# Performance work log

Measured on AMD Instinct MI355X. Metric: run time of the kernel, lower is better.

The kernel has to match this reference:

```python
import jax, jax.numpy as jnp
import numpy as np

B, T, H, W, D, NH, DEPTH, NCODES = 2, 16, 16, 16, 512, 8, 6, 1024
HW = H * W; DH = D // NH; KH = KW = 3; SIZE = KH * KW; MLP_DIM = 2 * D
NEG = -1e9


def _ln(x, g, b, eps=1e-5):
    m = jnp.mean(x, -1, keepdims=True)
    v = jnp.mean((x - m) ** 2, -1, keepdims=True)
    return (x - m) * jax.lax.rsqrt(v + eps) * g + b


def _rope(x, pos):
    # x: [N, h, T, dh]; half-split rotary embedding
    half = x.shape[-1] // 2
    freqs = 1.0 / (10000.0 ** (jnp.arange(half, dtype=jnp.float32) / half))
    ang = pos[:, None] * freqs[None]            # [T, half]
    cos = jnp.concatenate([jnp.cos(ang), jnp.cos(ang)], -1)
    sin = jnp.concatenate([jnp.sin(ang), jnp.sin(ang)], -1)
    rot = jnp.concatenate([-x[..., half:], x[..., :half]], -1)
    return x * cos + rot * sin


def setup_inputs() -> dict:
    key = jax.random.key(0)
    keys = iter(jax.random.split(key, 64))
    def p(shape, s=0.02):
        return (s * jax.random.normal(next(keys), shape)).astype(jnp.float32)
    inp = dict(
        codes=jax.random.randint(next(keys), (B, T, HW), 0, NCODES),
        emb_table=p((NCODES, D)),
        cls_token=p((1, 1, 1, D)),
        h_emb=p((1, 1, H, D)),
        w_emb=p((1, 1, W, D)),
        emb_norm_g=jnp.ones(D), emb_norm_b=jnp.zeros(D),
        sn_g=jnp.ones((DEPTH, D)), sn_b=jnp.zeros((DEPTH, D)),
        s_wq=p((DEPTH, D, D)), s_bq=jnp.zeros((DEPTH, D)),
        s_wk=p((DEPTH, D, D)), s_bk=jnp.zeros((DEPTH, D)),
        s_wv=p((DEPTH, D, D)), s_bv=jnp.zeros((DEPTH, D)),
        s_wo=p((DEPTH, D, D)), s_bo=jnp.zeros((DEPTH, D)),
        tn_g=jnp.ones((DEPTH, D)), tn_b=jnp.zeros((DEPTH, D)),
        t_wq=p((DEPTH, D, D)), t_bq=jnp.zeros((DEPTH, D)),
        t_wk=p((DEPTH, D, D)), t_bk=jnp.zeros((DEPTH, D)),
        t_wv=p((DEPTH, D, D)), t_bv=jnp.zeros((DEPTH, D)),
        t_wo=p((DEPTH, D, D)), t_bo=jnp.zeros((DEPTH, D)),
        mn_g=jnp.ones((DEPTH, D)), mn_b=jnp.zeros((DEPTH, D)),
        mlp_w1=p((DEPTH, D, MLP_DIM)), mlp_b1=jnp.zeros((DEPTH, MLP_DIM)),
        mlp_w2=p((DEPTH, MLP_DIM, D)), mlp_b2=jnp.zeros((DEPTH, D)),
        fn_g=jnp.ones(D), fn_b=jnp.zeros(D),
    )
    return inp


def reference(codes, emb_table, cls_token, h_emb, w_emb, emb_norm_g, emb_norm_b,
              sn_g, sn_b, s_wq, s_bq, s_wk, s_bk, s_wv, s_bv, s_wo, s_bo,
              tn_g, tn_b, t_wq, t_bq, t_wk, t_bk, t_wv, t_bv, t_wo, t_bo,
              mn_g, mn_b, mlp_w1, mlp_b1, mlp_w2, mlp_b2, fn_g, fn_b):
    T1 = T + 1
    emb = emb_table[codes]                                   # [B,T,HW,D]
    # positional embeddings exactly as torch repeat / repeat_interleave
    x = emb + jnp.tile(h_emb, (1, 1, W, 1)) + jnp.repeat(w_emb, H, axis=2)
    x = jnp.concatenate([x, jnp.broadcast_to(cls_token, (B, 1, HW, D))], axis=1)
    x = _ln(x, emb_norm_g, emb_norm_b)                       # [B,T1,HW,D]

    # temporal causal mask: True = masked
    tmask = jnp.triu(jnp.ones((T1, T1), dtype=bool), 1).at[-1, -1].set(True)
    # spatial out-of-bounds mask [H,W,SIZE] from unfold of ones with zero pad
    ones_pad = jnp.pad(jnp.ones((H, W), jnp.float32), 1)
    smask = jnp.stack([ones_pad[a:a + H, b:b + W]
                       for a in range(KH) for b in range(KW)], -1) == 0

    scale = 1.0 / jnp.sqrt(jnp.float32(DH))
    pos = jnp.arange(T1, dtype=jnp.float32)
    k_list, v_list = [], []
    attn_logits = None
    for i in range(DEPTH):
        # ---- spatial windowed attention on frames 0..T-1 ----
        xg = x[:, :-1].reshape(B, T, H, W, D)
        xn = _ln(xg, sn_g[i], sn_b[i])
        pad = jnp.pad(xn, ((0, 0), (0, 0), (1, 1), (1, 1), (0, 0)))
        nb = jnp.stack([pad[:, :, a:a + H, b:b + W]
                        for a in range(KH) for b in range(KW)], axis=4)  # [B,T,H,W,SIZE,D]
        q = (xn @ s_wq[i] + s_bq[i]).reshape(B, T, H, W, NH, DH)
        kk = (nb @ s_wk[i] + s_bk[i]).reshape(B, T, H, W, SIZE, NH, DH)
        vv = (nb @ s_wv[i] + s_bv[i]).reshape(B, T, H, W, SIZE, NH, DH)
        lg = jnp.einsum('btxynd,btxysnd->btxyns', q, kk) * scale
        lg = jnp.where(smask[None, None, :, :, None, :], NEG, lg)
        a_sp = jax.nn.softmax(lg, -1)
        o = jnp.einsum('btxyns,btxysnd->btxynd', a_sp, vv).reshape(B, T, H, W, D)
        o = o @ s_wo[i] + s_bo[i]
        x_sp = (o + xg).reshape(B, T, HW, D)                 # residual (drop_path=id, eval)
        xt = jnp.concatenate([x_sp, x[:, -1:]], axis=1)      # [B,T1,HW,D]

        # ---- temporal RoPE causal attention over T1 per spatial location ----
        s = xt.transpose(0, 2, 1, 3).reshape(B * HW, T1, D)
        sn_ = _ln(s, tn_g[i], tn_b[i])
        def heads(y):
            return y.reshape(B * HW, T1, NH, DH).transpose(0, 2, 1, 3)
        qt = _rope(heads(sn_ @ t_wq[i] + t_bq[i]), pos)
        kt = _rope(heads(sn_ @ t_wk[i] + t_bk[i]), pos)
        vt = heads(sn_ @ t_wv[i] + t_bv[i])
        lt = jnp.einsum('nhqd,nhkd->nhqk', qt, kt) * scale
        lt = jnp.where(tmask[None, None], NEG, lt)
        at = jax.nn.softmax(lt, -1)
        ot = jnp.einsum('nhqk,nhkd->nhqd', at, vt).transpose(0, 2, 1, 3).reshape(B * HW, T1, D)
        s = (ot @ t_wo[i] + t_bo[i]) + s
        xo = s.reshape(B, HW, T1, D).transpose(0, 2, 1, 3)   # [B,T1,HW,D]
        # average frame 0 over HW and broadcast back (as in torch code)
        xo = xo.at[:, 0].set(jnp.broadcast_to(xo[:, 0].mean(axis=1, keepdims=True), (B, HW, D)))
        attn_logits = lt.reshape(B, HW, NH, T1, T1)

        # ---- MLP (dim -> 2*dim, tanh, -> dim), dropout off in eval ----
        y = jnp.tanh(_ln(xo, mn_g[i], mn_b[i]) @ mlp_w1[i] + mlp_b1[i]) @ mlp_w2[i] + mlp_b2[i]
        x = y + xo
        k_list.append(kt[:, :, :-1, :])
        v_list.append(vt[:, :, :-1, :])

    return _ln(x, fn_g, fn_b), attn_logits, jnp.stack(k_list), jnp.stack(v_list)
```

## Files before the change

### kernel.cpp

```cpp
#include <hip/hip_runtime.h>
#include <hip/hip_bf16.h>
#include <math.h>

#define D_    512
#define NHH   8
#define DH_   64
#define T_    16
#define T1_   17
#define HWL   256
#define B__   2
#define NEGV  -1e9f

typedef __attribute__((ext_vector_type(8))) short short8;
typedef __attribute__((ext_vector_type(4))) short short4v;
typedef __attribute__((ext_vector_type(4))) float f32x4;
typedef __hip_bfloat16 bf16;

__device__ inline float wave_sum(float v){
  #pragma unroll
  for(int o=32;o>0;o>>=1) v += __shfl_xor(v,o,64);
  return v;
}
__device__ inline float b2f(unsigned short s){
  unsigned u = ((unsigned)s)<<16; float f; __builtin_memcpy(&f,&u,4); return f;
}
__device__ inline short f2bs(float f){
  bf16 h = __float2bfloat16(f); short s; __builtin_memcpy(&s,&h,2); return s;
}
__device__ inline void gload_lds16(const void* g, void* l){
  __builtin_amdgcn_global_load_lds((const __attribute__((address_space(1))) void*)g,
                                   (__attribute__((address_space(3))) void*)l, 16, 0, 0);
}

__global__ __launch_bounds__(256) void embed_ln_kernel(
    const int* __restrict__ codes, const float* __restrict__ emb,
    const float* __restrict__ cls, const float* __restrict__ hpos,
    const float* __restrict__ wpos, const float* __restrict__ g,
    const float* __restrict__ bta, bf16* __restrict__ X){
  int row  = blockIdx.x*4 + (threadIdx.x>>6);
  int lane = threadIdx.x & 63;
  int hw = row % HWL; int bt = row / HWL; int t = bt % T1_; int bb = bt / T1_;
  float v[8];
  if(t < T_){
    int code = codes[(bb*T_ + t)*HWL + hw];
    const float4* ep = (const float4*)(emb  + (size_t)code*D_);
    const float4* hp = (const float4*)(hpos + (size_t)(hw & 15)*D_);
    const float4* wp = (const float4*)(wpos + (size_t)(hw >> 4)*D_);
    float4 a0=ep[lane*2], a1=ep[lane*2+1];
    float4 h0=hp[lane*2], h1=hp[lane*2+1];
    float4 w0=wp[lane*2], w1=wp[lane*2+1];
    v[0]=a0.x+h0.x+w0.x; v[1]=a0.y+h0.y+w0.y; v[2]=a0.z+h0.z+w0.z; v[3]=a0.w+h0.w+w0.w;
    v[4]=a1.x+h1.x+w1.x; v[5]=a1.y+h1.y+w1.y; v[6]=a1.z+h1.z+w1.z; v[7]=a1.w+h1.w+w1.w;
  } else {
    const float4* cp = (const float4*)cls;
    float4 c0=cp[lane*2], c1=cp[lane*2+1];
    v[0]=c0.x; v[1]=c0.y; v[2]=c0.z; v[3]=c0.w; v[4]=c1.x; v[5]=c1.y; v[6]=c1.z; v[7]=c1.w;
  }
  float s=0;
  #pragma unroll
  for(int j=0;j<8;j++) s += v[j];
  s = wave_sum(s);
  float mean = s*(1.f/512.f);
  float s2=0;
  #pragma unroll
  for(int j=0;j<8;j++){ float d0=v[j]-mean; s2 += d0*d0; }
  s2 = wave_sum(s2);
  float inv = rsqrtf(s2*(1.f/512.f) + 1e-5f);
  const float4* g4 = (const float4*)g; const float4* b4 = (const float4*)bta;
  float4 gv=g4[lane*2], gw=g4[lane*2+1], bv=b4[lane*2], bw=b4[lane*2+1];
  short4v r0 = { f2bs((v[0]-mean)*inv*gv.x+bv.x), f2bs((v[1]-mean)*inv*gv.y+bv.y),
                 f2bs((v[2]-mean)*inv*gv.z+bv.z), f2bs((v[3]-mean)*inv*gv.w+bv.w) };
  short4v r1 = { f2bs((v[4]-mean)*inv*gw.x+bw.x), f2bs((v[5]-mean)*inv*gw.y+bw.y),
                 f2bs((v[6]-mean)*inv*gw.z+bw.z), f2bs((v[7]-mean)*inv*gw.w+bw.w) };
  bf16* o = X + (size_t)row*D_;
  *(short4v*)&o[lane*8]     = r0;
  *(short4v*)&o[lane*8 + 4] = r1;
}

__global__ __launch_bounds__(256) void ln_kernel(
    const bf16* __restrict__ in, float* __restrict__ out,
    const float* __restrict__ g, const float* __restrict__ bta,
    int c_rpb, int s_rpb){
  int row  = blockIdx.x*4 + (threadIdx.x>>6);
  int lane = threadIdx.x & 63;
  int bb = row / c_rpb; int rem = row - bb*c_rpb;
  short8 vv = *(const short8*)(in + ((size_t)bb*s_rpb + rem)*D_ + lane*8);
  float v[8]; float s=0;
  #pragma unroll
  for(int j=0;j<8;j++){ v[j] = b2f((unsigned short)vv[j]); s += v[j]; }
  s = wave_sum(s);
  float mean = s*(1.f/512.f);
  float s2=0;
  #pragma unroll
  for(int j=0;j<8;j++){ float d0=v[j]-mean; s2 += d0*d0; }
  s2 = wave_sum(s2);
  float inv = rsqrtf(s2*(1.f/512.f) + 1e-5f);
  const float4* g4 = (const float4*)g; const float4* b4 = (const float4*)bta;
  float4 gv=g4[lane*2], gw=g4[lane*2+1], bv=b4[lane*2], bw=b4[lane*2+1];
  float4 o0 = { (v[0]-mean)*inv*gv.x+bv.x, (v[1]-mean)*inv*gv.y+bv.y,
                (v[2]-mean)*inv*gv.z+bv.z, (v[3]-mean)*inv*gv.w+bv.w };
  float4 o1 = { (v[4]-mean)*inv*gw.x+bw.x, (v[5]-mean)*inv*gw.y+bw.y,
                (v[6]-mean)*inv*gw.z+bw.z, (v[7]-mean)*inv*gw.w+bw.w };
  float* o = out + (size_t)row*D_;
  *(float4*)&o[lane*8]     = o0;
  *(float4*)&o[lane*8 + 4] = o1;
}

__global__ __launch_bounds__(256) void ln_bf_kernel(
    const bf16* __restrict__ in, bf16* __restrict__ out,
    const float* __restrict__ g, const float* __restrict__ bta,
    int c_rpb, int s_rpb){
  int row  = blockIdx.x*4 + (threadIdx.x>>6);
  int lane = threadIdx.x & 63;
  int bb = row / c_rpb; int rem = row - bb*c_rpb;
  short8 vv = *(const short8*)(in + ((size_t)bb*s_rpb + rem)*D_ + lane*8);
  float v[8]; float s=0;
  #pragma unroll
  for(int j=0;j<8;j++){ v[j] = b2f((unsigned short)vv[j]); s += v[j]; }
  s = wave_sum(s);
  float mean = s*(1.f/512.f);
  float s2=0;
  #pragma unroll
  for(int j=0;j<8;j++){ float d0=v[j]-mean; s2 += d0*d0; }
  s2 = wave_sum(s2);
  float inv = rsqrtf(s2*(1.f/512.f) + 1e-5f);
  const float4* g4 = (const float4*)g; const float4* b4 = (const float4*)bta;
  float4 gv=g4[lane*2], gw=g4[lane*2+1], bv=b4[lane*2], bw=b4[lane*2+1];
  short4v r0 = { f2bs((v[0]-mean)*inv*gv.x+bv.x), f2bs((v[1]-mean)*inv*gv.y+bv.y),
                 f2bs((v[2]-mean)*inv*gv.z+bv.z), f2bs((v[3]-mean)*inv*gv.w+bv.w) };
  short4v r1 = { f2bs((v[4]-mean)*inv*gw.x+bw.x), f2bs((v[5]-mean)*inv*gw.y+bw.y),
                 f2bs((v[6]-mean)*inv*gw.z+bw.z), f2bs((v[7]-mean)*inv*gw.w+bw.w) };
  bf16* o = out + (size_t)row*D_;
  *(short4v*)&o[lane*8]     = r0;
  *(short4v*)&o[lane*8 + 4] = r1;
}

__global__ __launch_bounds__(256) void wconv_kernel(
    const float* sq, const float* sk, const float* sv, const float* so,
    const float* tq, const float* tk, const float* tv, const float* to,
    const float* w1, const float* w2, bf16* __restrict__ dst){
  __shared__ float sm[32][33];
  int z = blockIdx.z; int i = z/10, id = z - i*10;
  const size_t wo = (size_t)i*262144, mo = (size_t)i*524288;
  bf16* db = dst + (size_t)i*3145728;
  const float* src; bf16* d; int K, N;
  switch(id){
    case 0: src=sq+wo; d=db+0*262144;  K=512;  N=512;  break;
    case 1: src=sk+wo; d=db+1*262144;  K=512;  N=512;  break;
    case 2: src=sv+wo; d=db+2*262144;  K=512;  N=512;  break;
    case 3: src=so+wo; d=db+3*262144;  K=512;  N=512;  break;
    case 4: src=tq+wo; d=db+4*262144;  K=512;  N=512;  break;
    case 5: src=tk+wo; d=db+5*262144;  K=512;  N=512;  break;
    case 6: src=tv+wo; d=db+6*262144;  K=512;  N=512;  break;
    case 7: src=to+wo; d=db+7*262144;  K=512;  N=512;  break;
    case 8: src=w1+mo; d=db+2097152;   K=512;  N=1024; break;
    default:src=w2+mo; d=db+2621440;   K=1024; N=512;  break;
  }
  int n0 = blockIdx.x<<5, k0 = blockIdx.y<<5;
  if(n0 >= N || k0 >= K) return;
  int tx = threadIdx.x & 31, ty = threadIdx.x >> 5;
  #pragma unroll
  for(int j=0;j<4;j++) sm[ty+j*8][tx] = src[(size_t)(k0+ty+j*8)*N + n0+tx];
  __syncthreads();
  #pragma unroll
  for(int j=0;j<4;j++) d[(size_t)(n0+ty+j*8)*K + k0+tx] = __float2bfloat16(sm[tx][ty+j*8]);
}

template<int ACT, bool RES, bool OBF>
__global__ __launch_bounds__(256) void gemm_mfma(
    const bf16* __restrict__ A, const bf16* __restrict__ Wt,
    const float* __restrict__ bias, void* __restrict__ outp,
    const bf16* __restrict__ resid, int K, int N, int c_rpb, int o_rpb){
  __shared__ __align__(16) bf16 As[128*64];
  __shared__ __align__(16) bf16 Bs[128*64];
  const int tid  = threadIdx.x;
  const int lane = tid & 63;
  const int w    = tid >> 6;
  const int row0 = blockIdx.y << 7;
  const int col0 = blockIdx.x << 7;
  const int mb = (w>>1)*64, nb = (w&1)*64;
  size_t ga[4], gb[4];
  #pragma unroll
  for(int r=0;r<4;r++){
    int c = (r*4+w)*64 + lane;
    int rw = c>>3;
    int ks = (c&7) ^ (rw&7);
    ga[r] = (size_t)(row0+rw)*K + (ks<<3);
    gb[r] = (size_t)(col0+rw)*K + (ks<<3);
  }
  f32x4 acc[4][4] = {};
  for(int k0=0;k0<K;k0+=64){
    #pragma unroll
    for(int r=0;r<4;r++){
      gload_lds16(A  + ga[r] + k0, As + (size_t)(r*4+w)*512);
      gload_lds16(Wt + gb[r] + k0, Bs + (size_t)(r*4+w)*512);
    }
    __syncthreads();
    const short8* Av = (const short8*)As;
    const short8* Bv = (const short8*)Bs;
    #pragma unroll
    for(int kk=0;kk<2;kk++){
      const int slot = (lane>>4) + kk*4;
      short8 af[4], bfr[4];
      #pragma unroll
      for(int mi=0;mi<4;mi++){ int rw = mb + mi*16 + (lane&15); af[mi]  = Av[rw*8 + (slot ^ (rw&7))]; }
      #pragma unroll
      for(int ni=0;ni<4;ni++){ int rw = nb + ni*16 + (lane&15); bfr[ni] = Bv[rw*8 + (slot ^ (rw&7))]; }
      #pragma unroll
      for(int mi=0;mi<4;mi++)
        #pragma unroll
        for(int ni=0;ni<4;ni++)
          acc[mi][ni] = __builtin_amdgcn_mfma_f32_16x16x32_bf16(af[mi], bfr[ni], acc[mi][ni], 0,0,0);
    }
    __syncthreads();
  }
  #pragma unroll
  for(int mi=0;mi<4;mi++){
    #pragma unroll
    for(int r=0;r<4;r++){
      int row = row0 + mb + mi*16 + (lane>>4)*4 + r;
      int bb = row / c_rpb;
      size_t orow = (size_t)bb*o_rpb + (row - bb*c_rpb);
      #pragma unroll
      for(int ni=0;ni<4;ni++){
        int col = col0 + nb + ni*16 + (lane&15);
        float v = acc[mi][ni][r] + bias[col];
        if(ACT==1) v = tanhf(v);
        if(RES) v += __bfloat162float(resid[orow*(size_t)N + col]);
        if(OBF) ((bf16*)outp)[orow*(size_t)N + col] = __float2bfloat16(v);
        else    ((float*)outp)[orow*(size_t)N + col] = v;
      }
    }
  }
}

__global__ __launch_bounds__(256) void gemm_mfma64(
    const bf16* __restrict__ A, const bf16* __restrict__ Wt,
    const float* __restrict__ bias, bf16* __restrict__ outp,
    const bf16* __restrict__ resid, int K, int N, int c_rpb, int o_rpb){
  __shared__ __align__(16) bf16 As[2][64*64];
  __shared__ __align__(16) bf16 Bs[2][64*64];
  const int tid  = threadIdx.x;
  const int lane = tid & 63;
  const int w    = tid >> 6;
  const int row0 = blockIdx.y << 6;
  const int col0 = blockIdx.x << 6;
  const int mw = (w>>1)*32, nw = (w&1)*32;
  size_t ga[2], gb[2];
  #pragma unroll
  for(int r=0;r<2;r++){
    int c = (r*4+w)*64 + lane;
    int rw = c>>3;
    int ks = (c&7) ^ (rw&7);
    ga[r] = (size_t)(row0+rw)*K + (ks<<3);
    gb[r] = (size_t)(col0+rw)*K + (ks<<3);
  }
  f32x4 acc[2][2] = {};
  #pragma unroll
  for(int r=0;r<2;r++){
    gload_lds16(A  + ga[r], &As[0][(r*4+w)*512]);
    gload_lds16(Wt + gb[r], &Bs[0][(r*4+w)*512]);
  }
  __syncthreads();
  int cur = 0;
  for(int k0=0;k0<K;k0+=64){
    if(k0+64 < K){
      #pragma unroll
      for(int r=0;r<2;r++){
        gload_lds16(A  + ga[r] + k0+64, &As[cur^1][(r*4+w)*512]);
        gload_lds16(Wt + gb[r] + k0+64, &Bs[cur^1][(r*4+w)*512]);
      }
    }
    const short8* Av = (const short8*)As[cur];
    const short8* Bv = (const short8*)Bs[cur];
    #pragma unroll
    for(int kk=0;kk<2;kk++){
      const int slot = (lane>>4) + kk*4;
      short8 af[2], bfr[2];
      #pragma unroll
      for(int mi=0;mi<2;mi++){ int rw = mw + mi*16 + (lane&15); af[mi]  = Av[rw*8 + (slot ^ (rw&7))]; }
      #pragma unroll
      for(int ni=0;ni<2;ni++){ int rw = nw + ni*16 + (lane&15); bfr[ni] = Bv[rw*8 + (slot ^ (rw&7))]; }
      #pragma unroll
      for(int mi=0;mi<2;mi++)
        #pragma unroll
        for(int ni=0;ni<2;ni++)
          acc[mi][ni] = __builtin_amdgcn_mfma_f32_16x16x32_bf16(af[mi], bfr[ni], acc[mi][ni], 0,0,0);
    }
    __syncthreads();
    cur ^= 1;
  }
  #pragma unroll
  for(int mi=0;mi<2;mi++){
    #pragma unroll
    for(int r=0;r<4;r++){
      int row = row0 + mw + mi*16 + (lane>>4)*4 + r;
      int bb = row / c_rpb;
      size_t orow = (size_t)bb*o_rpb + (row - bb*c_rpb);
      #pragma unroll
      for(int ni=0;ni<2;ni++){
        int col = col0 + nw + ni*16 + (lane&15);
        float v = acc[mi][ni][r] + bias[col];
        v += __bfloat162float(resid[orow*(size_t)N + col]);
        outp[orow*(size_t)N + col] = __float2bfloat16(v);
      }
    }
  }
}

__global__ __launch_bounds__(256) void gemm_qkv(
    const bf16* __restrict__ A, const bf16* __restrict__ Wt,
    const float* __restrict__ bq, const float* __restrict__ bk, const float* __restrict__ bv,
    bf16* __restrict__ Qo, bf16* __restrict__ Ko, bf16* __restrict__ Vo){
  const int K = 512;
  __shared__ __align__(16) bf16 As[128*64];
  __shared__ __align__(16) bf16 Bs[128*64];
  const int tid  = threadIdx.x;
  const int lane = tid & 63;
  const int w    = tid >> 6;
  const int row0 = blockIdx.y << 7;
  const int col0 = blockIdx.x << 7;
  const int mb = (w>>1)*64, nb = (w&1)*64;
  size_t ga[4], gb[4];
  #pragma unroll
  for(int r=0;r<4;r++){
    int c = (r*4+w)*64 + lane;
    int rw = c>>3;
    int ks = (c&7) ^ (rw&7);
    ga[r] = (size_t)(row0+rw)*K + (ks<<3);
    gb[r] = (size_t)(col0+rw)*K + (ks<<3);
  }
  f32x4 acc[4][4] = {};
  for(int k0=0;k0<K;k0+=64){
    #pragma unroll
    for(int r=0;r<4;r++){
      gload_lds16(A  + ga[r] + k0, As + (size_t)(r*4+w)*512);
      gload_lds16(Wt + gb[r] + k0, Bs + (size_t)(r*4+w)*512);
    }
    __syncthreads();
    const short8* Av = (const short8*)As;
    const short8* Bv = (const short8*)Bs;
    #pragma unroll
    for(int kk=0;kk<2;kk++){
      const int slot = (lane>>4) + kk*4;
      short8 af[4], bfr[4];
      #pragma unroll
      for(int mi=0;mi<4;mi++){ int rw = mb + mi*16 + (lane&15); af[mi]  = Av[rw*8 + (slot ^ (rw&7))]; }
      #pragma unroll
      for(int ni=0;ni<4;ni++){ int rw = nb + ni*16 + (lane&15); bfr[ni] = Bv[rw*8 + (slot ^ (rw&7))]; }
      #pragma unroll
      for(int mi=0;mi<4;mi++)
        #pragma unroll
        for(int ni=0;ni<4;ni++)
          acc[mi][ni] = __builtin_amdgcn_mfma_f32_16x16x32_bf16(af[mi], bfr[ni], acc[mi][ni], 0,0,0);
    }
    __syncthreads();
  }
  const int sel = col0 >> 9;
  bf16* outp = (sel==0) ? Qo : (sel==1 ? Ko : Vo);
  const float* bp = (sel==0) ? bq : (sel==1 ? bk : bv);
  const int cb = col0 & 511;
  #pragma unroll
  for(int mi=0;mi<4;mi++){
    #pragma unroll
    for(int r=0;r<4;r++){
      int row = row0 + mb + mi*16 + (lane>>4)*4 + r;
      #pragma unroll
      for(int ni=0;ni<4;ni++){
        int col = cb + nb + ni*16 + (lane&15);
        outp[(size_t)row*512 + col] = __float2bfloat16(acc[mi][ni][r] + bp[col]);
      }
    }
  }
}

__global__ __launch_bounds__(256) void spatial_attn_kernel(
    const bf16* __restrict__ Q, const bf16* __restrict__ K,
    const bf16* __restrict__ V, bf16* __restrict__ O){
  int loc = blockIdx.x;
  int hw = loc & 255;
  int hh = hw >> 4, ww = hw & 15;
  int tid = threadIdx.x, lane = tid & 63, w = tid >> 6;
  int h = w*2 + (lane>>5);
  int j = lane & 31;
  size_t base = (size_t)loc*D_ + h*DH_ + 2*j;
  unsigned uq = *(const unsigned*)&Q[base];
  float q0 = b2f((unsigned short)uq), q1 = b2f((unsigned short)(uq>>16));
  float lg[9]; int nrow[9];
  #pragma unroll
  for(int s=0;s<9;s++){
    int a = s/3 - 1, b2_ = s%3 - 1;
    int nh = hh + a, nw = ww + b2_;
    bool ok = ((unsigned)nh < 16u) && ((unsigned)nw < 16u);
    nrow[s] = ok ? (loc - hw + (nh<<4) + nw) : -1;
    float p = 0.f;
    if(ok){
      unsigned uk = *(const unsigned*)&K[(size_t)nrow[s]*D_ + h*DH_ + 2*j];
      p = q0*b2f((unsigned short)uk) + q1*b2f((unsigned short)(uk>>16));
    }
    #pragma unroll
    for(int o=16;o>0;o>>=1) p += __shfl_xor(p, o, 64);
    lg[s] = ok ? p*0.125f : NEGV;
  }
  float m = lg[0];
  #pragma unroll
  for(int s=1;s<9;s++) m = fmaxf(m, lg[s]);
  float den = 0.f, wv[9];
  #pragma unroll
  for(int s=0;s<9;s++){ wv[s] = __expf(lg[s]-m); den += wv[s]; }
  float inv = 1.f/den;
  float a0 = 0.f, a1 = 0.f;
  #pragma unroll
  for(int s=0;s<9;s++){
    if(nrow[s] >= 0){
      unsigned uv = *(const unsigned*)&V[(size_t)nrow[s]*D_ + h*DH_ + 2*j];
      a0 += wv[s]*b2f((unsigned short)uv);
      a1 += wv[s]*b2f((unsigned short)(uv>>16));
    }
  }
  unsigned up = (unsigned)(unsigned short)f2bs(a0*inv) | ((unsigned)(unsigned short)f2bs(a1*inv) << 16);
  *(unsigned*)&O[base] = up;
}

__global__ __launch_bounds__(512) void fused_tattn(
    const bf16* __restrict__ Qb, const bf16* __restrict__ Kb, const bf16* __restrict__ Vb,
    bf16* __restrict__ O, float* __restrict__ kout, float* __restrict__ vout,
    float* __restrict__ ltout, int write_lt){
  __shared__ __align__(16) bf16 Qs[17*520];
  __shared__ __align__(16) bf16 Ks[17*520];
  __shared__ __align__(16) bf16 Vs[17*512];
  __shared__ float Ws[8][17][18];
  const int tid = threadIdx.x, w = tid>>6, lane = tid&63;
  const int hw = blockIdx.x & 255, b = blockIdx.x >> 8;
  const size_t tstr = (size_t)HWL*D_;
  const size_t rb0 = ((size_t)(b*T1_)*HWL + hw)*D_;
  for(int t=w; t<17; t+=8){
    size_t src = rb0 + (size_t)t*tstr + lane*8;
    *(short8*)&Qs[t*520 + lane*8] = *(const short8*)&Qb[src];
    *(short8*)&Ks[t*520 + lane*8] = *(const short8*)&Kb[src];
    *(short8*)&Vs[t*512 + lane*8] = *(const short8*)&Vb[src];
  }
  __syncthreads();
  {
    int i = lane & 31;
    float freq = __expf(-9.210340372f * (float)i * (1.f/32.f));
    bf16* P = (lane < 32) ? Qs : Ks;
    #pragma unroll
    for(int t=0;t<17;t++){
      float sn, cs; __sincosf((float)t*freq, &sn, &cs);
      int idx = t*520 + w*64 + i;
      float x1 = __bfloat162float(P[idx]);
      float x2 = __bfloat162float(P[idx+32]);
      P[idx]    = __float2bfloat16(x1*cs - x2*sn);
      P[idx+32] = __float2bfloat16(x2*cs + x1*sn);
    }
  }
  __syncthreads();
  {
    size_t eb = (((size_t)(b*HWL + hw)*NHH + w)*16)*64 + lane;
    #pragma unroll
    for(int t=0;t<16;t++){
      kout[eb + t*64] = __bfloat162float(Ks[t*520 + w*64 + lane]);
      vout[eb + t*64] = __bfloat162float(Vs[t*512 + w*64 + lane]);
    }
  }
  size_t lb = ((size_t)(b*HWL + hw)*NHH + w)*289;
  for(int p=lane; p<289; p+=64){
    int t = p/17, u = p - t*17;
    float d = 0.f;
    #pragma unroll
    for(int jj=0;jj<8;jj++){
      short8 qq = *(short8*)&Qs[t*520 + w*64 + jj*8];
      short8 kk = *(short8*)&Ks[u*520 + w*64 + jj*8];
      #pragma unroll
      for(int e=0;e<8;e++) d += b2f((unsigned short)qq[e]) * b2f((unsigned short)kk[e]);
    }
    bool masked = (u > t) || (t == 16 && u == 16);
    float lg = masked ? NEGV : d*0.125f;
    Ws[w][t][u] = lg;
    if(write_lt) ltout[lb + t*17 + u] = lg;
  }
  __syncthreads();
  if(lane < 17){
    float m = -1e30f;
    #pragma unroll
    for(int u=0;u<17;u++) m = fmaxf(m, Ws[w][lane][u]);
    float den = 0.f, e[17];
    #pragma unroll
    for(int u=0;u<17;u++){ e[u] = __expf(Ws[w][lane][u]-m); den += e[u]; }
    float inv = 1.f/den;
    #pragma unroll
    for(int u=0;u<17;u++) Ws[w][lane][u] = e[u]*inv;
  }
  __syncthreads();
  float Vr[17];
  #pragma unroll
  for(int u=0;u<17;u++) Vr[u] = __bfloat162float(Vs[u*512 + w*64 + lane]);
  #pragma unroll
  for(int t=0;t<17;t++){
    float acc = 0.f;
    #pragma unroll
    for(int u=0;u<17;u++) acc += Ws[w][t][u]*Vr[u];
    O[rb0 + (size_t)t*tstr + w*64 + lane] = __float2bfloat16(acc);
  }
}

__global__ __launch_bounds__(256) void avg_frame0_kernel(bf16* __restrict__ X){
  int b = blockIdx.x >> 3, c = blockIdx.x & 7;
  int ro = threadIdx.x >> 6, dd = threadIdx.x & 63;
  size_t base = ((size_t)(b*T1_)*HWL)*D_ + c*64 + dd;
  float acc = 0.f;
  for(int r=ro; r<256; r+=4) acc += __bfloat162float(X[base + (size_t)r*D_]);
  __shared__ float sm[4][64];
  sm[ro][dd] = acc;
  __syncthreads();
  float v = (sm[0][dd]+sm[1][dd]+sm[2][dd]+sm[3][dd])*(1.f/256.f);
  bf16 bv = __float2bfloat16(v);
  for(int r=ro; r<256; r+=4) X[base + (size_t)r*D_] = bv;
}

extern "C" void kernel_launch(void* const* d_in, const int* in_sizes, int n_in,
                              void* d_out, int out_size, void* d_ws, size_t ws_size,
                              hipStream_t stream){
  const int*   codes = (const int*)  d_in[0];
  const float* emb   = (const float*)d_in[1];
  const float* cls   = (const float*)d_in[2];
  const float* hpos  = (const float*)d_in[3];
  const float* wpos  = (const float*)d_in[4];
  const float* eng   = (const float*)d_in[5];
  const float* enb   = (const float*)d_in[6];
  const float* sn_g  = (const float*)d_in[7];
  const float* sn_b  = (const float*)d_in[8];
  const float* s_wq  = (const float*)d_in[9];
  const float* s_bq  = (const float*)d_in[10];
  const float* s_wk  = (const float*)d_in[11];
  const float* s_bk  = (const float*)d_in[12];
  const float* s_wv  = (const float*)d_in[13];
  const float* s_bv  = (const float*)d_in[14];
  const float* s_wo  = (const float*)d_in[15];
  const float* s_bo  = (const float*)d_in[16];
  const float* tn_g  = (const float*)d_in[17];
  const float* tn_b  = (const float*)d_in[18];
  const float* t_wq  = (const float*)d_in[19];
  const float* t_bq  = (const float*)d_in[20];
  const float* t_wk  = (const float*)d_in[21];
  const float* t_bk  = (const float*)d_in[22];
  const float* t_wv  = (const float*)d_in[23];
  const float* t_bv  = (const float*)d_in[24];
  const float* t_wo  = (const float*)d_in[25];
  const float* t_bo  = (const float*)d_in[26];
  const float* mn_g  = (const float*)d_in[27];
  const float* mn_b  = (const float*)d_in[28];
  const float* mw1   = (const float*)d_in[29];
  const float* mb1   = (const float*)d_in[30];
  const float* mw2   = (const float*)d_in[31];
  const float* mb2   = (const float*)d_in[32];
  const float* fn_g  = (const float*)d_in[33];
  const float* fn_b  = (const float*)d_in[34];

  const size_t NX = 4456448;
  bf16* Xb  = (bf16*)d_ws;
  bf16* XNb = Xb  + NX;
  bf16* Qb  = XNb + NX;
  bf16* Kb  = Qb  + NX;
  bf16* Vb  = Kb  + NX;
  bf16* Wt  = Vb  + NX;
  bf16* HIDb= Qb;

  float* out0 = (float*)d_out;
  float* out1 = out0 + NX;
  float* out2 = out1 + 1183744;
  float* out3 = out2 + 25165824;

  const int RS = B__*T_*HWL;
  const int RT = B__*T1_*HWL;
  dim3 gQs(12, 64);
  dim3 gQt(12, 68);
  dim3 g64s(8, 128);
  dim3 g64t(8, 136);
  dim3 gM1(8, 68);
  dim3 wcg(32, 32, 60);

  embed_ln_kernel<<<RT/4, 256, 0, stream>>>(codes, emb, cls, hpos, wpos, eng, enb, Xb);
  wconv_kernel<<<wcg,256,0,stream>>>(s_wq, s_wk, s_wv, s_wo, t_wq, t_wk, t_wv, t_wo, mw1, mw2, Wt);

  for(int i=0;i<6;i++){
    bf16* Wl = Wt + (size_t)i*3145728;
    ln_bf_kernel<<<RS/4,256,0,stream>>>(Xb, XNb, sn_g+i*D_, sn_b+i*D_, T_*HWL, T1_*HWL);
    gemm_qkv<<<gQs,256,0,stream>>>(XNb, Wl, s_bq+i*D_, s_bk+i*D_, s_bv+i*D_, Qb, Kb, Vb);
    spatial_attn_kernel<<<RS,256,0,stream>>>(Qb, Kb, Vb, XNb);
    gemm_mfma64<<<g64s,256,0,stream>>>(XNb, Wl+3*262144, s_bo+i*D_, Xb, Xb, 512, 512, T_*HWL, T1_*HWL);
    ln_bf_kernel<<<RT/4,256,0,stream>>>(Xb, XNb, tn_g+i*D_, tn_b+i*D_, T1_*HWL, T1_*HWL);
    gemm_qkv<<<gQt,256,0,stream>>>(XNb, Wl+4*262144, t_bq+i*D_, t_bk+i*D_, t_bv+i*D_, Qb, Kb, Vb);
    fused_tattn<<<512,512,0,stream>>>(Qb, Kb, Vb, XNb,
                                      out2+(size_t)i*4194304, out3+(size_t)i*4194304,
                                      out1, (i==5)?1:0);
    gemm_mfma64<<<g64t,256,0,stream>>>(XNb, Wl+7*262144, t_bo+i*D_, Xb, Xb, 512, 512, RT, RT);
    avg_frame0_kernel<<<16,256,0,stream>>>(Xb);
    ln_bf_kernel<<<RT/4,256,0,stream>>>(Xb, XNb, mn_g+i*D_, mn_b+i*D_, T1_*HWL, T1_*HWL);
    gemm_mfma<1,false,true ><<<gM1,256,0,stream>>>(XNb, Wl+2097152, mb1+i*1024, HIDb, nullptr, 512, 1024, RT, RT);
    gemm_mfma64<<<g64t,256,0,stream>>>(HIDb, Wl+2621440, mb2+i*D_, Xb, Xb, 1024, 512, RT, RT);
  }
  ln_kernel<<<RT/4,256,0,stream>>>(Xb, out0, fn_g, fn_b, T1_*HWL, T1_*HWL);
}
```

Measured before the change: 1.386 ms.

## Tile spatial attention per frame-head in LDS with XOR-swizzled staging

The spatial neighborhood attention kernel is restructured so that each block handles one (frame, head) pair. It stages the full 256x64 Q, K and V tiles into shared memory through swizzled async loads, and each thread then computes one pixel's 3x3 neighborhood attention from LDS. The old version launched one block per location and reloaded K and V rows from global memory for every neighbor, and the new layout is meant to remove that redundant traffic along with the cross-lane shuffle reductions. In exchange the grid shrinks to 256 blocks using 96KB of LDS each, which limits occupancy, and the output is written back through LDS for coalesced stores.

```diff
diff --git a/kernel.cpp b/kernel.cpp
--- a/kernel.cpp
+++ b/kernel.cpp
@@ -377,30 +377,47 @@
 __global__ __launch_bounds__(256) void spatial_attn_kernel(
     const bf16* __restrict__ Q, const bf16* __restrict__ K,
     const bf16* __restrict__ V, bf16* __restrict__ O){
-  int loc = blockIdx.x;
-  int hw = loc & 255;
-  int hh = hw >> 4, ww = hw & 15;
-  int tid = threadIdx.x, lane = tid & 63, w = tid >> 6;
-  int h = w*2 + (lane>>5);
-  int j = lane & 31;
-  size_t base = (size_t)loc*D_ + h*DH_ + 2*j;
-  unsigned uq = *(const unsigned*)&Q[base];
-  float q0 = b2f((unsigned short)uq), q1 = b2f((unsigned short)(uq>>16));
+  __shared__ __align__(16) bf16 Qs[256*64];
+  __shared__ __align__(16) bf16 Ks[256*64];
+  __shared__ __align__(16) bf16 Vs[256*64];
+  const int f = blockIdx.x >> 3, h = blockIdx.x & 7;
+  const int tid = threadIdx.x;
+  const size_t base = ((size_t)f*256)*512 + h*64;
+  #pragma unroll
+  for(int j=0;j<8;j++){
+    int c = tid + j*256;
+    int r = c >> 3, sl = c & 7;
+    size_t src = base + (size_t)r*512 + ((sl ^ (r&7))<<3);
+    gload_lds16(Q + src, Qs + (size_t)c*8);
+    gload_lds16(K + src, Ks + (size_t)c*8);
+    gload_lds16(V + src, Vs + (size_t)c*8);
+  }
+  __syncthreads();
+  const int hh = tid >> 4, ww = tid & 15;
+  const short8* Qv = (const short8*)Qs;
+  const short8* Kv = (const short8*)Ks;
+  const short8* Vv = (const short8*)Vs;
+  short8 q[8];
+  #pragma unroll
+  for(int j=0;j<8;j++) q[j] = Qv[tid*8 + (j ^ (tid&7))];
   float lg[9]; int nrow[9];
   #pragma unroll
   for(int s=0;s<9;s++){
     int a = s/3 - 1, b2_ = s%3 - 1;
     int nh = hh + a, nw = ww + b2_;
     bool ok = ((unsigned)nh < 16u) && ((unsigned)nw < 16u);
-    nrow[s] = ok ? (loc - hw + (nh<<4) + nw) : -1;
-    float p = 0.f;
+    int nr = (nh<<4) + nw;
+    nrow[s] = ok ? nr : -1;
+    float d = 0.f;
     if(ok){
-      unsigned uk = *(const unsigned*)&K[(size_t)nrow[s]*D_ + h*DH_ + 2*j];
-      p = q0*b2f((unsigned short)uk) + q1*b2f((unsigned short)(uk>>16));
-    }
-    #pragma unroll
-    for(int o=16;o>0;o>>=1) p += __shfl_xor(p, o, 64);
-    lg[s] = ok ? p*0.125f : NEGV;
+      #pragma unroll
+      for(int j=0;j<8;j++){
+        short8 kk = Kv[nr*8 + (j ^ (nr&7))];
+        #pragma unroll
+        for(int e=0;e<8;e++) d += b2f((unsigned short)q[j][e]) * b2f((unsigned short)kk[e]);
+      }
+    }
+    lg[s] = ok ? d*0.125f : NEGV;
   }
   float m = lg[0];
   #pragma unroll
@@ -409,17 +426,32 @@
   #pragma unroll
   for(int s=0;s<9;s++){ wv[s] = __expf(lg[s]-m); den += wv[s]; }
   float inv = 1.f/den;
-  float a0 = 0.f, a1 = 0.f;
-  #pragma unroll
-  for(int s=0;s<9;s++){
-    if(nrow[s] >= 0){
-      unsigned uv = *(const unsigned*)&V[(size_t)nrow[s]*D_ + h*DH_ + 2*j];
-      a0 += wv[s]*b2f((unsigned short)uv);
-      a1 += wv[s]*b2f((unsigned short)(uv>>16));
-    }
-  }
-  unsigned up = (unsigned)(unsigned short)f2bs(a0*inv) | ((unsigned)(unsigned short)f2bs(a1*inv) << 16);
-  *(unsigned*)&O[base] = up;
+  #pragma unroll
+  for(int s=0;s<9;s++) wv[s] *= inv;
+  #pragma unroll
+  for(int j=0;j<8;j++){
+    float acc8[8] = {};
+    #pragma unroll
+    for(int s=0;s<9;s++){
+      if(nrow[s] >= 0){
+        short8 vvv = Vv[nrow[s]*8 + (j ^ (nrow[s]&7))];
+        #pragma unroll
+        for(int e=0;e<8;e++) acc8[e] += wv[s]*b2f((unsigned short)vvv[e]);
+      }
+    }
+    short8 ovec;
+    #pragma unroll
+    for(int e=0;e<8;e++) ovec[e] = f2bs(acc8[e]);
+    *(short8*)&Qs[(tid*8 + (j ^ (tid&7)))*8] = ovec;
+  }
+  __syncthreads();
+  #pragma unroll
+  for(int j=0;j<8;j++){
+    int c = tid + j*256;
+    int r = c >> 3, sl = c & 7;
+    short8 ovec = Qv[r*8 + ((sl ^ (r&7)))];
+    *(short8*)&O[base + (size_t)r*512 + (sl<<3)] = ovec;
+  }
 }
 
 __global__ __launch_bounds__(512) void fused_tattn(
@@ -588,7 +620,7 @@
     bf16* Wl = Wt + (size_t)i*3145728;
     ln_bf_kernel<<<RS/4,256,0,stream>>>(Xb, XNb, sn_g+i*D_, sn_b+i*D_, T_*HWL, T1_*HWL);
     gemm_qkv<<<gQs,256,0,stream>>>(XNb, Wl, s_bq+i*D_, s_bk+i*D_, s_bv+i*D_, Qb, Kb, Vb);
-    spatial_attn_kernel<<<RS,256,0,stream>>>(Qb, Kb, Vb, XNb);
+    spatial_attn_kernel<<<256,256,0,stream>>>(Qb, Kb, Vb, XNb);
     gemm_mfma64<<<g64s,256,0,stream>>>(XNb, Wl+3*262144, s_bo+i*D_, Xb, Xb, 512, 512, T_*HWL, T1_*HWL);
     ln_bf_kernel<<<RT/4,256,0,stream>>>(Xb, XNb, tn_g+i*D_, tn_b+i*D_, T1_*HWL, T1_*HWL);
     gemm_qkv<<<gQt,256,0,stream>>>(XNb, Wl+4*262144, t_bq+i*D_, t_bk+i*D_, t_bv+i*D_, Qb, Kb, Vb);
```

Result: faster. 1.295 ms (-6.6%).
